# Optimization experiments

Hardware: AMD Instinct MI355X
Metric: run time of the kernel (lower is better)

The kernel has to match this reference:

```python
import jax, jax.numpy as jnp
import numpy as np

STEP = 0.175
K = 128  # static bin cap; randn data at step 0.175 needs ~70 bins, so clipping is a no-op


def _bin_idx(x, step):
    # pd.cut(data, bins=arange(floor(min), ceil(max)+step, step)): interval (b[i], b[i+1]]
    # -> idx = ceil((x - lower)/step) - 1. Labels (bin midpoints) are bijective with idx,
    # so all downstream Counter/entropy math can run on integer bin indices directly.
    lower = jnp.floor(jnp.min(x))
    return jnp.clip(jnp.ceil((x - lower) / step) - 1, 0, K - 1).astype(jnp.int32)


def _row_entropy(codes):
    # plug-in Shannon entropy (natural log, like scipy.stats.entropy) per row:
    # H = log n - mean_j log(count of codes[j]); counts via sort + searchsorted runs
    s = jnp.sort(codes, axis=1)
    left = jax.vmap(lambda r: jnp.searchsorted(r, r, side='left'))(s)
    right = jax.vmap(lambda r: jnp.searchsorted(r, r, side='right'))(s)
    cnt = (right - left).astype(jnp.float32)
    return jnp.log(jnp.float32(codes.shape[1])) - jnp.mean(jnp.log(cnt), axis=1)


def _soft_ce(logits, target):
    # F.cross_entropy with soft targets, reduction='mean' (mean over batch)
    return jnp.mean(-jnp.sum(target * jax.nn.log_softmax(logits, -1), axis=-1))


def _kl_mean(logits, target):
    # F.kl_div(log_softmax(logits), target, reduction='mean') -> mean over ALL elements
    logp = jax.nn.log_softmax(logits, -1)
    return jnp.mean(target * (jnp.log(target) - logp))


def _H_out(logits, target):
    return _soft_ce(logits, target) - _kl_mean(logits, target)


def setup_inputs() -> dict:
    key = jax.random.key(0)
    ks = jax.random.split(key, 8)
    B, D = 4096, 1024
    return {
        'data': jax.random.normal(ks[0], (B, 3 * D), jnp.float32),
        'data1': jax.random.normal(ks[1], (B, D), jnp.float32),
        'data2': jax.random.normal(ks[2], (B, D), jnp.float32),
        'data3': jax.random.normal(ks[3], (B, D), jnp.float32),
        'output1': jax.random.normal(ks[4], (B, D), jnp.float32),
        'output2': jax.random.normal(ks[5], (B, D), jnp.float32),
        'output3': jax.random.normal(ks[6], (B, D), jnp.float32),
        'output': jax.random.normal(ks[7], (B, 3 * D), jnp.float32),
    }


def reference(data, data1, data2, data3, output1, output2, output3, output):
    cat = lambda xs: jnp.concatenate(xs, axis=1)
    mse = 0.5 * jnp.mean((data - output) ** 2)

    # discretized histogram/entropy path runs on .detach()'d numpy in torch -> stop_gradient
    i1 = _bin_idx(jax.lax.stop_gradient(data1), STEP)
    i2 = _bin_idx(jax.lax.stop_gradient(data2), STEP)
    i3 = _bin_idx(jax.lax.stop_gradient(data3), STEP)

    H_d1 = jnp.mean(_row_entropy(i1))
    H_d2 = jnp.mean(_row_entropy(i2))
    H_d3 = jnp.mean(_row_entropy(i3))

    p1 = jax.nn.softmax(data1, -1)
    p2 = jax.nn.softmax(data2, -1)
    p3 = jax.nn.softmax(data3, -1)
    H_o1 = _H_out(output1, p1)
    H_o2 = _H_out(output2, p2)
    H_o3 = _H_out(output3, p3)

    H_1 = H_d1 - H_o1
    H_2 = H_d2 - H_o2
    H_3 = H_d3 - H_o3

    # ave_joint_entropy over padded label matrices == joint entropy of (idx_x, idx_y) pairs
    # (equal column counts -> pad_matrices is a no-op; labels<->indices are bijective)
    H_in_13 = jnp.mean(_row_entropy(i1 * K + i3))
    H_in_23 = jnp.mean(_row_entropy(i2 * K + i3))
    H_in_12 = jnp.mean(_row_entropy(i1 * K + i2))

    H_o13 = _H_out(cat([output1, output3]), jax.nn.softmax(cat([data1, data3]), -1))
    H_o23 = _H_out(cat([output2, output3]), jax.nn.softmax(cat([data2, data3]), -1))
    H_o12 = _H_out(cat([output1, output2]), jax.nn.softmax(cat([data1, data2]), -1))

    H_MI13 = (H_o1 + H_o3 - H_o13) - (H_d1 + H_d3 - H_in_13)
    H_MI23 = (H_o2 + H_o3 - H_o23) - (H_d2 + H_d3 - H_in_23)
    H_MI12 = (H_o1 + H_o2 - H_o12) - (H_d1 + H_d2 - H_in_12)

    # per-row conditional MI I(x1; x2 | x3) = H(1,3)+H(2,3)-H(3)-H(1,2,3), SUMMED over rows
    c123 = (i1 * K + i2) * K + i3
    cmi_rows = (_row_entropy(i1 * K + i3) + _row_entropy(i2 * K + i3)
                - _row_entropy(i3) - _row_entropy(c123))
    data_mu = jnp.sum(cmi_rows)

    H_o123 = _H_out(cat([output1, output2, output3]),
                    jax.nn.softmax(cat([data1, data2, data3]), -1))
    label_cmi = H_o23 - H_o3 + H_o13 - H_o123
    CMI = label_cmi - data_mu

    return 0.9 * mse + 0.1 * (H_1 ** 2 + H_2 ** 2 + H_3 ** 2
                              + H_MI13 ** 2 + H_MI23 ** 2 + H_MI12 ** 2 + CMI ** 2)
```

## Files before the change

kernel.cpp:

```cpp
#include <hip/hip_runtime.h>
#include <stdint.h>

#define ROWS 4096
#define NCOL 1024
#define NT 256
#define NBANK 64
#define BSTRIDE 32

#define NB 72
#define ROWB 76
#define PAIRW (NB * (ROWB / 4))
#define TRIW 2048
#define T23_BASE PAIRW
#define T31_BASE (2 * PAIRW)
#define TRI_BASE (3 * PAIRW)
#define TABW (3 * PAIRW + TRIW)


__device__ __forceinline__ uint32_t f2ord(float f) {
  uint32_t b = __float_as_uint(f);
  return (b & 0x80000000u) ? ~b : (b | 0x80000000u);
}
__device__ __forceinline__ float ord2f(uint32_t u) {
  uint32_t b = (u & 0x80000000u) ? (u & 0x7FFFFFFFu) : ~u;
  return __uint_as_float(b);
}

__global__ __launch_bounds__(256) void k_pre(
    const float4* __restrict__ d1, const float4* __restrict__ d2,
    const float4* __restrict__ d3, uint32_t* __restrict__ minb) {
  __shared__ float sred[4];
  const int t = threadIdx.x;
  const float4* p = (blockIdx.y == 0) ? d1 : (blockIdx.y == 1) ? d2 : d3;
  const int n4 = ROWS * NCOL / 4;
  float lm = 1e30f;
  for (int i = blockIdx.x * 256 + t; i < n4; i += gridDim.x * 256) {
    float4 v = p[i];
    lm = fminf(lm, fminf(fminf(v.x, v.y), fminf(v.z, v.w)));
  }
  for (int o = 32; o > 0; o >>= 1) lm = fminf(lm, __shfl_down(lm, o, 64));
  if ((t & 63) == 0) sred[t >> 6] = lm;
  __syncthreads();
  if (t == 0) {
    lm = fminf(fminf(sred[0], sred[1]), fminf(sred[2], sred[3]));
    atomicMax(&minb[blockIdx.y], ~f2ord(lm));
  }
}

__device__ __noinline__ void hslow(uint32_t* __restrict__ tri, uint32_t key,
                                   uint32_t slot) {
  slot = (slot + 1u) & (TRIW - 1u);
  for (;;) {
    uint32_t cur = tri[slot];
    if ((cur >> 11) == key) { atomicAdd((unsigned int*)&tri[slot], 1u); return; }
    if (cur == 0u) {
      uint32_t old = atomicCAS((unsigned int*)&tri[slot], 0u, (key << 11) | 1u);
      if (old == 0u) return;
      if ((old >> 11) == key) { atomicAdd((unsigned int*)&tri[slot], 1u); return; }
    }
    slot = (slot + 1u) & (TRIW - 1u);
  }
}

__device__ __forceinline__ uint32_t bini(float x, float low) {
  return (uint32_t)min(max((int)ceilf((x - low) * (1.0f / 0.175f)) - 1, 0),
                       NB - 1);
}

__global__ __launch_bounds__(NT) void k_row(
    const float* __restrict__ d1, const float* __restrict__ d2,
    const float* __restrict__ d3, const float* __restrict__ o1,
    const float* __restrict__ o2, const float* __restrict__ o3,
    const float4* __restrict__ data, const float4* __restrict__ outp,
    const uint32_t* __restrict__ minb, float* __restrict__ acc) {
  __shared__ uint32_t tab[TABW];
  __shared__ float sA[4][12];
  __shared__ float sB[4][8];
  const int r = blockIdx.x, t = threadIdx.x;
  float* bank = acc + (r & (NBANK - 1)) * BSTRIDE;

#pragma unroll
  for (int i = t; i < TABW / 4; i += NT) ((uint4*)tab)[i] = make_uint4(0, 0, 0, 0);

  const float low1 = floorf(ord2f(~minb[0]));
  const float low2 = floorf(ord2f(~minb[1]));
  const float low3 = floorf(ord2f(~minb[2]));

  const size_t off = (size_t)r * NCOL;
  const float4 x1 = ((const float4*)(d1 + off))[t];
  const float4 x2 = ((const float4*)(d2 + off))[t];
  const float4 x3 = ((const float4*)(d3 + off))[t];
  const float xd[3][4] = {{x1.x, x1.y, x1.z, x1.w},
                          {x2.x, x2.y, x2.z, x2.w},
                          {x3.x, x3.y, x3.z, x3.w}};
  uint32_t b1[4], b2[4], b3[4];
#pragma unroll
  for (int u = 0; u < 4; ++u) {
    b1[u] = bini(xd[0][u], low1);
    b2[u] = bini(xd[1][u], low2);
    b3[u] = bini(xd[2][u], low3);
  }
  __syncthreads();

#pragma unroll
  for (int u = 0; u < 4; ++u) {
    const uint32_t i12 = b1[u] * ROWB + b2[u];
    const uint32_t i23 = b2[u] * ROWB + b3[u];
    const uint32_t i31 = b3[u] * ROWB + b1[u];
    atomicAdd((unsigned int*)&tab[i12 >> 2], 1u << ((i12 & 3u) * 8u));
    atomicAdd((unsigned int*)&tab[T23_BASE + (i23 >> 2)], 1u << ((i23 & 3u) * 8u));
    atomicAdd((unsigned int*)&tab[T31_BASE + (i31 >> 2)], 1u << ((i31 & 3u) * 8u));
  }
  uint32_t key[4], slot[4], old[4];
#pragma unroll
  for (int u = 0; u < 4; ++u) {
    key[u] = (b1[u] << 14) | (b2[u] << 7) | b3[u];
    slot[u] = (key[u] * 2654435761u) >> 21;
    old[u] = atomicCAS((unsigned int*)&tab[TRI_BASE + slot[u]], 0u,
                       (key[u] << 11) | 1u);
  }
#pragma unroll
  for (int u = 0; u < 4; ++u) {
    if (old[u] != 0u) {
      if ((old[u] >> 11) == key[u])
        atomicAdd((unsigned int*)&tab[TRI_BASE + slot[u]], 1u);
      else
        hslow(tab + TRI_BASE, key[u], slot[u]);
    }
  }

  float ms = 0.f;
  {
    const float4* pa = data + (size_t)r * 768;
    const float4* pb = outp + (size_t)r * 768;
#pragma unroll
    for (int u = 0; u < 3; ++u) {
      float4 a0 = pa[t + u * NT], bq = pb[t + u * NT];
      float dx = a0.x - bq.x, dy = a0.y - bq.y, dz = a0.z - bq.z, dw = a0.w - bq.w;
      ms += dx * dx + dy * dy + dz * dz + dw * dw;
    }
  }

  const float4 y1 = ((const float4*)(o1 + off))[t];
  const float4 y2 = ((const float4*)(o2 + off))[t];
  const float4 y3 = ((const float4*)(o3 + off))[t];
  const float xo[3][4] = {{y1.x, y1.y, y1.z, y1.w},
                          {y2.x, y2.y, y2.z, y2.w},
                          {y3.x, y3.y, y3.z, y3.w}};
  float v[12];
#pragma unroll
  for (int k = 0; k < 3; ++k) {
    float E = 0.f, F = 0.f, G = 0.f, LE = 0.f;
#pragma unroll
    for (int u = 0; u < 4; ++u) {
      float w = __expf(xd[k][u]);
      E += w;
      F += w * xd[k][u];
      G += w * xo[k][u];
      LE += __expf(xo[k][u]);
    }
    v[k * 4 + 0] = E; v[k * 4 + 1] = F; v[k * 4 + 2] = G; v[k * 4 + 3] = LE;
  }
#pragma unroll
  for (int o = 32; o > 0; o >>= 1)
#pragma unroll
    for (int j = 0; j < 12; ++j) v[j] += __shfl_down(v[j], o, 64);
  if ((t & 63) == 0)
#pragma unroll
    for (int j = 0; j < 12; ++j) sA[t >> 6][j] = v[j];
  __syncthreads();

  float p[8] = {0.f, 0.f, 0.f, 0.f, 0.f, 0.f, 0.f, 0.f};
  p[7] = ms;
  if (t < 3 * NB) {
    const int tbl = t / NB, row = t - tbl * NB;
    const int pidx = (tbl == 0) ? 3 : (tbl == 1) ? 5 : 4;
    const uint32_t base = (uint32_t)tbl * PAIRW + (uint32_t)row * (ROWB / 4);
    uint32_t rowsum = 0;
    float pl = 0.f;
#pragma unroll
    for (int w = 0; w < 18; ++w) {
      uint32_t vv = tab[base + w];
      if (vv) {
        uint32_t s2 = (vv & 0x00FF00FFu) + ((vv >> 8) & 0x00FF00FFu);
        rowsum += (s2 + (s2 >> 16)) & 0xFFFFu;
#pragma unroll
        for (int bq = 0; bq < 4; ++bq) {
          uint32_t c = (vv >> (8 * bq)) & 255u;
          if (c > 1u) { float fc = (float)c; pl += fc * __logf(fc); }
        }
      }
    }
    p[pidx] = pl;
    if (rowsum > 1u) { float fr = (float)rowsum; p[tbl] = fr * __logf(fr); }
  }
#pragma unroll
  for (int i = t; i < TRIW / 4; i += NT) {
    uint4 e = ((const uint4*)(tab + TRI_BASE))[i];
    uint32_t c0 = e.x & 0x7FFu, c1 = e.y & 0x7FFu, c2 = e.z & 0x7FFu,
             c3 = e.w & 0x7FFu;
    if (c0 > 1u) { float fc = (float)c0; p[6] += fc * __logf(fc); }
    if (c1 > 1u) { float fc = (float)c1; p[6] += fc * __logf(fc); }
    if (c2 > 1u) { float fc = (float)c2; p[6] += fc * __logf(fc); }
    if (c3 > 1u) { float fc = (float)c3; p[6] += fc * __logf(fc); }
  }
#pragma unroll
  for (int o = 32; o > 0; o >>= 1)
#pragma unroll
    for (int j = 0; j < 8; ++j) p[j] += __shfl_down(p[j], o, 64);
  if ((t & 63) == 0)
#pragma unroll
    for (int j = 0; j < 8; ++j) sB[t >> 6][j] = p[j];
  __syncthreads();

  if (t == 0) {
    float s[8];
#pragma unroll
    for (int j = 0; j < 8; ++j)
      s[j] = sB[0][j] + sB[1][j] + sB[2][j] + sB[3][j];
#pragma unroll
    for (int j = 0; j < 7; ++j) atomicAdd(&bank[1 + j], s[j]);
    atomicAdd(&bank[0], s[7]);

    double E[3], F[3], G[3], L[3];
#pragma unroll
    for (int k = 0; k < 3; ++k) {
      E[k] = (double)sA[0][k*4+0] + sA[1][k*4+0] + sA[2][k*4+0] + sA[3][k*4+0];
      F[k] = (double)sA[0][k*4+1] + sA[1][k*4+1] + sA[2][k*4+1] + sA[3][k*4+1];
      G[k] = (double)sA[0][k*4+2] + sA[1][k*4+2] + sA[2][k*4+2] + sA[3][k*4+2];
      L[k] = (double)sA[0][k*4+3] + sA[1][k*4+3] + sA[2][k*4+3] + sA[3][k*4+3];
    }
    const int masks[7] = {1, 2, 4, 5, 6, 3, 7};
#pragma unroll
    for (int c = 0; c < 7; ++c) {
      double Z = 0, Fs = 0, Gs = 0, LZ = 0;
      for (int k = 0; k < 3; ++k)
        if (masks[c] & (1 << k)) { Z += E[k]; Fs += F[k]; Gs += G[k]; LZ += L[k]; }
      double T = Fs / Z - log(Z);
      double A = -(Gs / Z) + log(LZ);
      atomicAdd(&bank[8 + c], (float)A);
      atomicAdd(&bank[15 + c], (float)T);
    }
  }
}

__global__ void k_final(const float* __restrict__ acc, float* __restrict__ out) {
  const int t = threadIdx.x;
  double q[22];
#pragma unroll
  for (int i = 0; i < 22; ++i) q[i] = (double)acc[t * BSTRIDE + i];
#pragma unroll
  for (int o = 32; o > 0; o >>= 1)
#pragma unroll
    for (int i = 0; i < 22; ++i) q[i] += __shfl_down(q[i], o, 64);
  if (t != 0) return;

  const double logn = log(1024.0);
  const double Rn = 4096.0 * 1024.0;
  double Hd1 = logn - q[1] / Rn, Hd2 = logn - q[2] / Rn, Hd3 = logn - q[3] / Rn;
  double Hin12 = logn - q[4] / Rn, Hin13 = logn - q[5] / Rn, Hin23 = logn - q[6] / Rn;
  double data_mu = (q[3] + q[7] - q[5] - q[6]) / 1024.0;

  auto hout = [](double A, double T, double D) {
    return (1.0 - 1.0 / D) * A / 4096.0 - T / (4096.0 * D);
  };
  double Ho1 = hout(q[8], q[15], 1024.0);
  double Ho2 = hout(q[9], q[16], 1024.0);
  double Ho3 = hout(q[10], q[17], 1024.0);
  double Ho13 = hout(q[11], q[18], 2048.0);
  double Ho23 = hout(q[12], q[19], 2048.0);
  double Ho12 = hout(q[13], q[20], 2048.0);
  double Ho123 = hout(q[14], q[21], 3072.0);

  double H1 = Hd1 - Ho1, H2 = Hd2 - Ho2, H3 = Hd3 - Ho3;
  double MI13 = (Ho1 + Ho3 - Ho13) - (Hd1 + Hd3 - Hin13);
  double MI23 = (Ho2 + Ho3 - Ho23) - (Hd2 + Hd3 - Hin23);
  double MI12 = (Ho1 + Ho2 - Ho12) - (Hd1 + Hd2 - Hin12);
  double label_cmi = Ho23 - Ho3 + Ho13 - Ho123;
  double CMI = label_cmi - data_mu;
  double mse = 0.5 * q[0] / (4096.0 * 3072.0);
  out[0] = (float)(0.9 * mse +
                   0.1 * (H1 * H1 + H2 * H2 + H3 * H3 + MI13 * MI13 +
                          MI23 * MI23 + MI12 * MI12 + CMI * CMI));
}

extern "C" void kernel_launch(void* const* d_in, const int* in_sizes, int n_in,
                              void* d_out, int out_size, void* d_ws, size_t ws_size,
                              hipStream_t stream) {
  const float* data  = (const float*)d_in[0];
  const float* data1 = (const float*)d_in[1];
  const float* data2 = (const float*)d_in[2];
  const float* data3 = (const float*)d_in[3];
  const float* out1  = (const float*)d_in[4];
  const float* out2  = (const float*)d_in[5];
  const float* out3  = (const float*)d_in[6];
  const float* outp  = (const float*)d_in[7];
  float* acc = (float*)d_ws;
  uint32_t* minb = (uint32_t*)((float*)d_ws + NBANK * BSTRIDE);

  hipMemsetAsync(acc, 0, NBANK * BSTRIDE * sizeof(float) + 3 * sizeof(uint32_t),
                 stream);
  k_pre<<<dim3(256, 3), 256, 0, stream>>>((const float4*)data1,
                                          (const float4*)data2,
                                          (const float4*)data3, minb);
  k_row<<<ROWS, NT, 0, stream>>>(data1, data2, data3, out1, out2, out3,
                                 (const float4*)data, (const float4*)outp,
                                 minb, acc);
  k_final<<<1, 64, 0, stream>>>(acc, (float*)d_out);
}
```

Before: 253.6 us.

## Shrink triple hash table, raise occupancy, parallelize per-row epilogue across lanes

Cuts the shared-memory triple hash table from 2048 to 1536 slots, with slot scaled by 3/4 and the probe wrapping explicitly, and adds a launch-bounds occupancy hint of 7 blocks. Hoists the output-row loads above the hashing atomics so their latency overlaps. Replaces the serial double-precision thread-0 epilogue with float math spread over 16 lanes, each issuing its own atomic. This lowers LDS use and the serial tail, at the cost of a higher hash load factor (more probing) and reduced precision in the per-row entropy terms.

```diff
diff --git a/kernel.cpp b/kernel.cpp
--- a/kernel.cpp
+++ b/kernel.cpp
@@ -10,7 +10,7 @@
 #define NB 72
 #define ROWB 76
 #define PAIRW (NB * (ROWB / 4))
-#define TRIW 2048
+#define TRIW 1536
 #define T23_BASE PAIRW
 #define T31_BASE (2 * PAIRW)
 #define TRI_BASE (3 * PAIRW)
@@ -49,8 +49,9 @@
 
 __device__ __noinline__ void hslow(uint32_t* __restrict__ tri, uint32_t key,
                                    uint32_t slot) {
-  slot = (slot + 1u) & (TRIW - 1u);
   for (;;) {
+    ++slot;
+    if (slot == TRIW) slot = 0;
     uint32_t cur = tri[slot];
     if ((cur >> 11) == key) { atomicAdd((unsigned int*)&tri[slot], 1u); return; }
     if (cur == 0u) {
@@ -58,7 +59,6 @@
       if (old == 0u) return;
       if ((old >> 11) == key) { atomicAdd((unsigned int*)&tri[slot], 1u); return; }
     }
-    slot = (slot + 1u) & (TRIW - 1u);
   }
 }
 
@@ -67,7 +67,7 @@
                        NB - 1);
 }
 
-__global__ __launch_bounds__(NT) void k_row(
+__global__ __launch_bounds__(NT, 7) void k_row(
     const float* __restrict__ d1, const float* __restrict__ d2,
     const float* __restrict__ d3, const float* __restrict__ o1,
     const float* __restrict__ o2, const float* __restrict__ o3,
@@ -111,11 +111,17 @@
     atomicAdd((unsigned int*)&tab[T23_BASE + (i23 >> 2)], 1u << ((i23 & 3u) * 8u));
     atomicAdd((unsigned int*)&tab[T31_BASE + (i31 >> 2)], 1u << ((i31 & 3u) * 8u));
   }
+
+  const float4 y1 = ((const float4*)(o1 + off))[t];
+  const float4 y2 = ((const float4*)(o2 + off))[t];
+  const float4 y3 = ((const float4*)(o3 + off))[t];
+
   uint32_t key[4], slot[4], old[4];
 #pragma unroll
   for (int u = 0; u < 4; ++u) {
     key[u] = (b1[u] << 14) | (b2[u] << 7) | b3[u];
-    slot[u] = (key[u] * 2654435761u) >> 21;
+    uint32_t h = (key[u] * 2654435761u) >> 21;
+    slot[u] = (h * 3u) >> 2;
     old[u] = atomicCAS((unsigned int*)&tab[TRI_BASE + slot[u]], 0u,
                        (key[u] << 11) | 1u);
   }
@@ -141,9 +147,6 @@
     }
   }
 
-  const float4 y1 = ((const float4*)(o1 + off))[t];
-  const float4 y2 = ((const float4*)(o2 + off))[t];
-  const float4 y3 = ((const float4*)(o3 + off))[t];
   const float xo[3][4] = {{y1.x, y1.y, y1.z, y1.w},
                           {y2.x, y2.y, y2.z, y2.w},
                           {y3.x, y3.y, y3.z, y3.w}};
@@ -194,7 +197,6 @@
     p[pidx] = pl;
     if (rowsum > 1u) { float fr = (float)rowsum; p[tbl] = fr * __logf(fr); }
   }
-#pragma unroll
   for (int i = t; i < TRIW / 4; i += NT) {
     uint4 e = ((const uint4*)(tab + TRI_BASE))[i];
     uint32_t c0 = e.x & 0x7FFu, c1 = e.y & 0x7FFu, c2 = e.z & 0x7FFu,
@@ -213,33 +215,32 @@
     for (int j = 0; j < 8; ++j) sB[t >> 6][j] = p[j];
   __syncthreads();
 
-  if (t == 0) {
-    float s[8];
-#pragma unroll
-    for (int j = 0; j < 8; ++j)
-      s[j] = sB[0][j] + sB[1][j] + sB[2][j] + sB[3][j];
-#pragma unroll
-    for (int j = 0; j < 7; ++j) atomicAdd(&bank[1 + j], s[j]);
-    atomicAdd(&bank[0], s[7]);
-
-    double E[3], F[3], G[3], L[3];
-#pragma unroll
-    for (int k = 0; k < 3; ++k) {
-      E[k] = (double)sA[0][k*4+0] + sA[1][k*4+0] + sA[2][k*4+0] + sA[3][k*4+0];
-      F[k] = (double)sA[0][k*4+1] + sA[1][k*4+1] + sA[2][k*4+1] + sA[3][k*4+1];
-      G[k] = (double)sA[0][k*4+2] + sA[1][k*4+2] + sA[2][k*4+2] + sA[3][k*4+2];
-      L[k] = (double)sA[0][k*4+3] + sA[1][k*4+3] + sA[2][k*4+3] + sA[3][k*4+3];
-    }
-    const int masks[7] = {1, 2, 4, 5, 6, 3, 7};
-#pragma unroll
-    for (int c = 0; c < 7; ++c) {
-      double Z = 0, Fs = 0, Gs = 0, LZ = 0;
+  if (t < 16) {
+    if (t < 7) {
+      const int masks[7] = {1, 2, 4, 5, 6, 3, 7};
+      const int m = masks[t];
+      float Z = 0.f, Fs = 0.f, Gs = 0.f, LZ = 0.f;
+#pragma unroll
       for (int k = 0; k < 3; ++k)
-        if (masks[c] & (1 << k)) { Z += E[k]; Fs += F[k]; Gs += G[k]; LZ += L[k]; }
-      double T = Fs / Z - log(Z);
-      double A = -(Gs / Z) + log(LZ);
-      atomicAdd(&bank[8 + c], (float)A);
-      atomicAdd(&bank[15 + c], (float)T);
+        if (m & (1 << k)) {
+#pragma unroll
+          for (int w = 0; w < 4; ++w) {
+            Z += sA[w][k * 4 + 0];
+            Fs += sA[w][k * 4 + 1];
+            Gs += sA[w][k * 4 + 2];
+            LZ += sA[w][k * 4 + 3];
+          }
+        }
+      const float rZ = 1.0f / Z;
+      const float T = Fs * rZ - __logf(Z);
+      const float A = -(Gs * rZ) + __logf(LZ);
+      atomicAdd(&bank[8 + t], A);
+      atomicAdd(&bank[15 + t], T);
+    } else if (t < 15) {
+      const int j = t - 8;
+      atomicAdd(&bank[1 + j], sB[0][j] + sB[1][j] + sB[2][j] + sB[3][j]);
+    } else {
+      atomicAdd(&bank[0], sB[0][7] + sB[1][7] + sB[2][7] + sB[3][7]);
     }
   }
 }
```

Result: faster. 242.5 us (-4.4%).
